# Kernel optimization log

Hardware: AMD Instinct MI355X
Metric: run time of the kernel (lower is better)

## Reference

```python
import jax, jax.numpy as jnp
import numpy as np
import math

D_MODEL, N_HEAD, N_KV_HEAD, MAX_LEN = 2048, 32, 8, 2048
D_K = D_MODEL // N_HEAD
BASE = 10000.0
B, T = 2, 2048


def _rope_tables(seq_len):
    # matches torch Rotary: cos/sin of shape [seq_len, D_K], repeat_interleave(2) over freq dim
    inv_freq = 1.0 / (BASE ** (jnp.arange(0, D_K, 2, dtype=jnp.float32) / D_K))
    t = jnp.arange(seq_len, dtype=jnp.float32)[:, None] * inv_freq  # [T, D_K/2]
    cos = jnp.repeat(jnp.cos(t), 2, axis=-1)  # [T, D_K]
    sin = jnp.repeat(jnp.sin(t), 2, axis=-1)
    return cos, sin


def _rotate_half(x):
    # faithful to source: x1 = even lanes, x2 = odd lanes, concat([-x2, x1], -1)
    x1, x2 = x[..., ::2], x[..., 1::2]
    return jnp.concatenate([-x2, x1], axis=-1)


def _apply_rope(x, cos, sin):
    return x * cos + _rotate_half(x) * sin


def setup_inputs() -> dict:
    key = jax.random.key(0)
    ks = jax.random.split(key, 5)
    s = 1.0 / math.sqrt(D_MODEL)
    x = jax.random.normal(ks[0], (B, T, D_MODEL), dtype=jnp.float32)
    Wq = jax.random.normal(ks[1], (D_MODEL, N_HEAD * D_K), dtype=jnp.float32) * s
    Wk = jax.random.normal(ks[2], (D_MODEL, N_KV_HEAD * D_K), dtype=jnp.float32) * s
    Wv = jax.random.normal(ks[3], (D_MODEL, N_KV_HEAD * D_K), dtype=jnp.float32) * s
    Wo = jax.random.normal(ks[4], (N_HEAD * D_K, D_MODEL), dtype=jnp.float32) * s
    mask = jnp.tril(jnp.ones((T, T), dtype=bool))  # causal
    return {"x": x, "mask": mask, "Wq": Wq, "Wk": Wk, "Wv": Wv, "Wo": Wo}


def reference(x, mask, Wq, Wk, Wv, Wo):
    b, t, _ = x.shape
    g = N_HEAD // N_KV_HEAD
    q = (x @ Wq).reshape(b, t, N_HEAD, D_K).transpose(0, 2, 1, 3)      # [B,H,T,d]
    k = (x @ Wk).reshape(b, t, N_KV_HEAD, D_K).transpose(0, 2, 1, 3)   # [B,Hkv,T,d]
    v = (x @ Wv).reshape(b, t, N_KV_HEAD, D_K).transpose(0, 2, 1, 3)
    cos, sin = _rope_tables(t)
    q = _apply_rope(q, cos, sin)
    k = _apply_rope(k, cos, sin)  # rope before/after repeat is identical per-head
    # grouped attention: q head h attends kv head h // g (repeat_interleave semantics)
    qg = q.reshape(b, N_KV_HEAD, g, t, D_K)
    scores = jnp.einsum("bkgtd,bksd->bkgts", qg, k) / math.sqrt(D_K)
    neg = jnp.finfo(scores.dtype).min
    scores = jnp.where(mask[None, None, None, :, :], scores, neg)
    attn = jax.nn.softmax(scores, axis=-1)
    out = jnp.einsum("bkgts,bksd->bkgtd", attn, v)
    out = out.reshape(b, N_HEAD, t, D_K).transpose(0, 2, 1, 3).reshape(b, t, N_HEAD * D_K)
    return out @ Wo
```

## Files before the change

### kernel.cpp

```cpp
#include <hip/hip_runtime.h>
#include <cstdint>
#include <cstddef>

typedef unsigned short u16;
typedef __attribute__((ext_vector_type(8))) short bf16x8;
typedef __attribute__((ext_vector_type(8))) unsigned short u16x8;
typedef __attribute__((ext_vector_type(4))) unsigned short u16x4;
typedef __attribute__((ext_vector_type(4))) float f32x4;

__device__ __forceinline__ unsigned short f2bf(float f) {
    union { float f; uint32_t u; } c; c.f = f;
    uint32_t u = c.u + 0x7fffu + ((c.u >> 16) & 1u);
    return (unsigned short)(u >> 16);
}
__device__ __forceinline__ float bf2f(unsigned short h) {
    union { uint32_t u; float f; } c; c.u = ((uint32_t)h) << 16;
    return c.f;
}
__device__ __forceinline__ uint32_t pkbf(float a, float b) {
    union { float f; uint32_t u; } x, y; x.f = a; y.f = b;
    return ((x.u + 0x8000u) >> 16) | ((y.u + 0x8000u) & 0xFFFF0000u);
}

#define GLDS16(g, l)                                                               \
    __builtin_amdgcn_global_load_lds((const __attribute__((address_space(1))) void*)(g), \
                                     (__attribute__((address_space(3))) void*)(l), 16, 0, 0)

__global__ __launch_bounds__(256) void cvt_x(const float* __restrict__ src,
                                             u16* __restrict__ dst) {
    int i = blockIdx.x * 256 + threadIdx.x;
    const float4* s = (const float4*)src + (size_t)i * 2;
    float4 a = s[0], b = s[1];
    u16x8 o;
    o[0] = f2bf(a.x); o[1] = f2bf(a.y); o[2] = f2bf(a.z); o[3] = f2bf(a.w);
    o[4] = f2bf(b.x); o[5] = f2bf(b.y); o[6] = f2bf(b.z); o[7] = f2bf(b.w);
    *(u16x8*)(dst + (size_t)i * 8) = o;
}

__global__ __launch_bounds__(256) void tcvt(const float* __restrict__ src,
                                            u16* __restrict__ dst, int C) {
    __shared__ u16 tile[32][33];
    const int t = threadIdx.x;
    const int bx = blockIdx.x, by = blockIdx.y;
    const int tr = t >> 3, tc = (t & 7) << 2;
    float4 f = *(const float4*)&src[(size_t)(by * 32 + tr) * C + bx * 32 + tc];
    tile[tr][tc + 0] = f2bf(f.x); tile[tr][tc + 1] = f2bf(f.y);
    tile[tr][tc + 2] = f2bf(f.z); tile[tr][tc + 3] = f2bf(f.w);
    __syncthreads();
    u16x4 o;
    o[0] = tile[tc + 0][tr]; o[1] = tile[tc + 1][tr];
    o[2] = tile[tc + 2][tr]; o[3] = tile[tc + 3][tr];
    *(u16x4*)&dst[(size_t)(bx * 32 + tr) * 2048 + by * 32 + tc] = o;
}

__global__ __launch_bounds__(256) void tcvt3(const float* __restrict__ Wq,
                                             const float* __restrict__ Wk,
                                             const float* __restrict__ Wv,
                                             u16* __restrict__ dst) {
    __shared__ u16 tile[32][33];
    const int t = threadIdx.x;
    const int bxg = blockIdx.x, by = blockIdx.y;
    const float* src; int C, nb; u16* dbase;
    if (bxg < 64)      { src = Wq; C = 2048; nb = bxg;      dbase = dst; }
    else if (bxg < 80) { src = Wk; C = 512;  nb = bxg - 64; dbase = dst + (size_t)2048 * 2048; }
    else               { src = Wv; C = 512;  nb = bxg - 80; dbase = dst + (size_t)2560 * 2048; }
    const int tr = t >> 3, tc = (t & 7) << 2;
    float4 f = *(const float4*)&src[(size_t)(by * 32 + tr) * C + nb * 32 + tc];
    tile[tr][tc + 0] = f2bf(f.x); tile[tr][tc + 1] = f2bf(f.y);
    tile[tr][tc + 2] = f2bf(f.z); tile[tr][tc + 3] = f2bf(f.w);
    __syncthreads();
    u16x4 o;
    o[0] = tile[tc + 0][tr]; o[1] = tile[tc + 1][tr];
    o[2] = tile[tc + 2][tr]; o[3] = tile[tc + 3][tr];
    *(u16x4*)&dbase[(size_t)(nb * 32 + tr) * 2048 + by * 32 + tc] = o;
}

template <int MODE>
__global__ __launch_bounds__(256) void gemm2(const u16* __restrict__ A,
                                             const u16* __restrict__ Bt,
                                             u16* __restrict__ oq, u16* __restrict__ ok,
                                             u16* __restrict__ ov, float* __restrict__ of) {
    __shared__ u16 As[128 * 32];
    __shared__ u16 Bs[128 * 32];
    const int t = threadIdx.x, w = t >> 6, lane = t & 63;
    const int l15 = lane & 15, quad = lane >> 4;
    const int m0 = blockIdx.y << 7, n0 = blockIdx.x << 7;
    const int K = 2048;
    const int c0 = w * 2, c1 = c0 + 1;
    const int ar0 = c0 * 16 + (lane >> 2), ar1 = c1 * 16 + (lane >> 2);
    const int ac = (lane & 3) << 3;
    const u16* Ap0 = A + (size_t)(m0 + ar0) * K + ac;
    const u16* Ap1 = A + (size_t)(m0 + ar1) * K + ac;
    const u16* Bp0 = Bt + (size_t)(n0 + ar0) * K + ac;
    const u16* Bp1 = Bt + (size_t)(n0 + ar1) * K + ac;
    const int wm = (w >> 1) << 6, wn = (w & 1) << 6;

    f32x4 acc[4][4] = {};

    for (int k0 = 0; k0 < K; k0 += 32) {
        GLDS16(Ap0 + k0, &As[c0 * 512]);
        GLDS16(Ap1 + k0, &As[c1 * 512]);
        GLDS16(Bp0 + k0, &Bs[c0 * 512]);
        GLDS16(Bp1 + k0, &Bs[c1 * 512]);
        __syncthreads();
        bf16x8 a[4], bfr[4];
#pragma unroll
        for (int mt = 0; mt < 4; ++mt)
            a[mt] = *(bf16x8*)&As[(wm + mt * 16 + l15) * 32 + quad * 8];
#pragma unroll
        for (int nt = 0; nt < 4; ++nt)
            bfr[nt] = *(bf16x8*)&Bs[(wn + nt * 16 + l15) * 32 + quad * 8];
#pragma unroll
        for (int mt = 0; mt < 4; ++mt)
#pragma unroll
            for (int nt = 0; nt < 4; ++nt)
                acc[mt][nt] = __builtin_amdgcn_mfma_f32_16x16x32_bf16(a[mt], bfr[nt], acc[mt][nt], 0, 0, 0);
        __syncthreads();
    }

    if constexpr (MODE == 0) {
        const int colbase = n0 + wn;
        const bool isv = (colbase >= 2560);
        float iv[4];
        if (!isv) {
#pragma unroll
            for (int nt = 0; nt < 4; ++nt)
                iv[nt] = exp2f(-0.4152410118609253f * (float)(nt * 8 + (l15 >> 1)));
        }
        const int map1 = (quad << 4) | ((2 * l15 + 1) & 15);
        const int map2 = (quad << 4) | ((2 * l15) & 15);
        const bool lo = (l15 < 8);
#pragma unroll
        for (int mt = 0; mt < 4; ++mt)
#pragma unroll
            for (int r = 0; r < 4; ++r) {
                const int row = m0 + wm + mt * 16 + quad * 4 + r;
                float v0 = acc[mt][0][r], v1 = acc[mt][1][r];
                float v2 = acc[mt][2][r], v3 = acc[mt][3][r];
                float o0 = v0, o1 = v1, o2 = v2, o3 = v3;
                if (!isv) {
                    float g1a = __shfl(v0, map1), g1b = __shfl(v1, map1);
                    float g1c = __shfl(v2, map1), g1d = __shfl(v3, map1);
                    float g2a = __shfl(v0, map2), g2b = __shfl(v1, map2);
                    float g2c = __shfl(v2, map2), g2d = __shfl(v3, map2);
                    float p0 = lo ? g1a : g1b;
                    float p1 = lo ? g1c : g1d;
                    float p2 = lo ? g2a : g2b;
                    float p3 = lo ? g2c : g2d;
                    const float tt = (float)(row & 2047);
                    float sn, cs;
                    __sincosf(tt * iv[0], &sn, &cs); o0 = v0 * cs - p0 * sn;
                    __sincosf(tt * iv[1], &sn, &cs); o1 = v1 * cs - p1 * sn;
                    __sincosf(tt * iv[2], &sn, &cs); o2 = v2 * cs + p2 * sn;
                    __sincosf(tt * iv[3], &sn, &cs); o3 = v3 * cs + p3 * sn;
                }
                float o[4] = {o0, o1, o2, o3};
                if (colbase < 2048) {
#pragma unroll
                    for (int nt = 0; nt < 4; ++nt)
                        oq[(size_t)row * 2048 + colbase + nt * 16 + l15] = f2bf(o[nt]);
                } else if (colbase < 2560) {
#pragma unroll
                    for (int nt = 0; nt < 4; ++nt)
                        ok[(size_t)row * 512 + colbase - 2048 + nt * 16 + l15] = f2bf(o[nt]);
                } else {
#pragma unroll
                    for (int nt = 0; nt < 4; ++nt)
                        ov[(size_t)(colbase - 2560 + nt * 16 + l15) * 4096 + row] = f2bf(o[nt]);
                }
            }
    } else {
#pragma unroll
        for (int mt = 0; mt < 4; ++mt)
#pragma unroll
            for (int nt = 0; nt < 4; ++nt)
#pragma unroll
                for (int r = 0; r < 4; ++r) {
                    int row = m0 + wm + mt * 16 + quad * 4 + r;
                    int col = n0 + wn + nt * 16 + l15;
                    of[(size_t)row * 2048 + col] = acc[mt][nt][r];
                }
    }
}

__global__ __launch_bounds__(256, 3) void attn4(const u16* __restrict__ q,
                                                const u16* __restrict__ k,
                                                const u16* __restrict__ vT,
                                                u16* __restrict__ att) {
    __shared__ u16 Ks[64 * 72];
    __shared__ u16 Vt[64 * 72];
    __shared__ u16 Pw[4][16 * 72];

    const int t = threadIdx.x, w = t >> 6, lane = t & 63;
    const int l15 = lane & 15, quad = lane >> 4;
    const int bx = blockIdx.x, kvh = blockIdx.y, b = blockIdx.z;
    const int h = kvh * 4 + w;
    const size_t rowbase = (size_t)b * 2048;
    const int sr = t >> 2, sd = (t & 3) << 4;
    u16* Pq = &Pw[w][0];
    const float SC = 0.125f * 1.4426950408889634f;

    const u16* kbase = &k[(rowbase + sr) * 512 + kvh * 64 + sd];
    const u16* vbase = &vT[(size_t)(kvh * 64 + sr) * 4096 + rowbase + sd];

    for (int grp = 0; grp < 2; ++grp) {
        const int g = grp ? (63 - bx) : bx;
        const int qbase = g * 32;
        const int ntiles = (g >> 1) + 1;

        bf16x8 aq[2][2];
#pragma unroll
        for (int mt = 0; mt < 2; ++mt)
#pragma unroll
            for (int kc = 0; kc < 2; ++kc)
                aq[mt][kc] = *(const bf16x8*)&q[(rowbase + qbase + mt * 16 + l15) * 2048 +
                                               h * 64 + kc * 32 + quad * 8];

        f32x4 acc[2][4] = {};
        float m_i[2] = {-INFINITY, -INFINITY};
        float l_i[2] = {0.f, 0.f};

        u16x8 pk0 = *(const u16x8*)kbase;
        u16x8 pk1 = *(const u16x8*)(kbase + 8);
        u16x8 pv0 = *(const u16x8*)vbase;
        u16x8 pv1 = *(const u16x8*)(vbase + 8);

        for (int kb = 0; kb < ntiles; ++kb) {
            __syncthreads();
            *(u16x8*)&Ks[sr * 72 + sd]     = pk0;
            *(u16x8*)&Ks[sr * 72 + sd + 8] = pk1;
            *(u16x8*)&Vt[sr * 72 + sd]     = pv0;
            *(u16x8*)&Vt[sr * 72 + sd + 8] = pv1;
            if (kb + 1 < ntiles) {
                const u16* kp = kbase + (size_t)(kb + 1) * 64 * 512;
                pk0 = *(const u16x8*)kp;
                pk1 = *(const u16x8*)(kp + 8);
                const u16* vp = vbase + (size_t)(kb + 1) * 64;
                pv0 = *(const u16x8*)vp;
                pv1 = *(const u16x8*)(vp + 8);
            }
            __syncthreads();

            f32x4 st[2][4] = {};
#pragma unroll
            for (int kt = 0; kt < 4; ++kt) {
                bf16x8 ak0 = *(bf16x8*)&Ks[(kt * 16 + l15) * 72 + quad * 8];
                bf16x8 ak1 = *(bf16x8*)&Ks[(kt * 16 + l15) * 72 + 32 + quad * 8];
                st[0][kt] = __builtin_amdgcn_mfma_f32_16x16x32_bf16(ak0, aq[0][0], st[0][kt], 0, 0, 0);
                st[0][kt] = __builtin_amdgcn_mfma_f32_16x16x32_bf16(ak1, aq[0][1], st[0][kt], 0, 0, 0);
                st[1][kt] = __builtin_amdgcn_mfma_f32_16x16x32_bf16(ak0, aq[1][0], st[1][kt], 0, 0, 0);
                st[1][kt] = __builtin_amdgcn_mfma_f32_16x16x32_bf16(ak1, aq[1][1], st[1][kt], 0, 0, 0);
            }
            const bool diag = (kb == ntiles - 1);

#pragma unroll
            for (int mt = 0; mt < 2; ++mt) {
                float sv[16];
#pragma unroll
                for (int kt = 0; kt < 4; ++kt)
#pragma unroll
                    for (int r = 0; r < 4; ++r) sv[kt * 4 + r] = st[mt][kt][r] * SC;
                if (diag) {
                    const int qg = qbase + mt * 16 + l15;
#pragma unroll
                    for (int kt = 0; kt < 4; ++kt)
#pragma unroll
                        for (int r = 0; r < 4; ++r) {
                            int key = kb * 64 + kt * 16 + quad * 4 + r;
                            if (key > qg) sv[kt * 4 + r] = -INFINITY;
                        }
                }
                float mx = sv[0];
#pragma unroll
                for (int i = 1; i < 16; ++i) mx = fmaxf(mx, sv[i]);
                mx = fmaxf(mx, __shfl_xor(mx, 16));
                mx = fmaxf(mx, __shfl_xor(mx, 32));
                float mnew = fmaxf(m_i[mt], mx);
                float sum = 0.f;
#pragma unroll
                for (int i = 0; i < 16; ++i) {
                    sv[i] = __builtin_amdgcn_exp2f(sv[i] - mnew);
                    sum += sv[i];
                }
                sum += __shfl_xor(sum, 16);
                sum += __shfl_xor(sum, 32);
                float alpha = __builtin_amdgcn_exp2f(m_i[mt] - mnew);
                l_i[mt] = l_i[mt] * alpha + sum;
                m_i[mt] = mnew;

#pragma unroll
                for (int kt = 0; kt < 4; ++kt) {
                    uint2 uu;
                    uu.x = pkbf(sv[kt * 4 + 0], sv[kt * 4 + 1]);
                    uu.y = pkbf(sv[kt * 4 + 2], sv[kt * 4 + 3]);
                    *(uint2*)&Pq[l15 * 72 + kt * 16 + quad * 4] = uu;
                }
                bf16x8 bp0 = *(bf16x8*)&Pq[l15 * 72 + quad * 8];
                bf16x8 bp1 = *(bf16x8*)&Pq[l15 * 72 + 32 + quad * 8];

#pragma unroll
                for (int dt = 0; dt < 4; ++dt) {
                    bf16x8 av0 = *(bf16x8*)&Vt[(dt * 16 + l15) * 72 + quad * 8];
                    bf16x8 av1 = *(bf16x8*)&Vt[(dt * 16 + l15) * 72 + 32 + quad * 8];
#pragma unroll
                    for (int r = 0; r < 4; ++r) acc[mt][dt][r] *= alpha;
                    acc[mt][dt] = __builtin_amdgcn_mfma_f32_16x16x32_bf16(av0, bp0, acc[mt][dt], 0, 0, 0);
                    acc[mt][dt] = __builtin_amdgcn_mfma_f32_16x16x32_bf16(av1, bp1, acc[mt][dt], 0, 0, 0);
                }
            }
        }

#pragma unroll
        for (int mt = 0; mt < 2; ++mt) {
            float inv = 1.0f / l_i[mt];
            size_t row = rowbase + qbase + mt * 16 + l15;
#pragma unroll
            for (int dt = 0; dt < 4; ++dt) {
                uint2 uu;
                uu.x = pkbf(acc[mt][dt][0] * inv, acc[mt][dt][1] * inv);
                uu.y = pkbf(acc[mt][dt][2] * inv, acc[mt][dt][3] * inv);
                *(uint2*)&att[row * 2048 + h * 64 + dt * 16 + quad * 4] = uu;
            }
        }
    }
}

extern "C" void kernel_launch(void* const* d_in, const int* in_sizes, int n_in,
                              void* d_out, int out_size, void* d_ws, size_t ws_size,
                              hipStream_t stream) {
    const float* x  = (const float*)d_in[0];
    const float* Wq = (const float*)d_in[2];
    const float* Wk = (const float*)d_in[3];
    const float* Wv = (const float*)d_in[4];
    const float* Wo = (const float*)d_in[5];
    float* out = (float*)d_out;

    u16* xb = (u16*)d_out;

    u16* q     = (u16*)d_ws;
    u16* kk    = q + (size_t)4096 * 2048;
    u16* vt    = kk + (size_t)4096 * 512;
    u16* wqkvt = vt + (size_t)4096 * 512;
    u16* att   = wqkvt;
    u16* wot   = kk;

    cvt_x<<<4096, 256, 0, stream>>>(x, xb);
    tcvt3<<<dim3(96, 64), 256, 0, stream>>>(Wq, Wk, Wv, wqkvt);
    gemm2<0><<<dim3(24, 32), 256, 0, stream>>>(xb, wqkvt, q, kk, vt, nullptr);
    attn4<<<dim3(32, 8, 2), 256, 0, stream>>>(q, kk, vt, att);
    tcvt<<<dim3(64, 64), 256, 0, stream>>>(Wo, wot, 2048);
    gemm2<1><<<dim3(16, 32), 256, 0, stream>>>(att, wot, nullptr, nullptr, nullptr, out);
}
```

Measured before the change: 332.4 us.

## Process 64-query tiles per wave with lazy softmax rescaling in attention

```diff
diff --git a/kernel.cpp b/kernel.cpp
--- a/kernel.cpp
+++ b/kernel.cpp
@@ -20,6 +20,11 @@
 __device__ __forceinline__ uint32_t pkbf(float a, float b) {
     union { float f; uint32_t u; } x, y; x.f = a; y.f = b;
     return ((x.u + 0x8000u) >> 16) | ((y.u + 0x8000u) & 0xFFFF0000u);
+}
+__device__ __forceinline__ uint32_t cvtpk(float a, float b) {
+    uint32_t r;
+    asm("v_cvt_pk_bf16_f32 %0, %1, %2" : "=v"(r) : "v"(a), "v"(b));
+    return r;
 }
 
 #define GLDS16(g, l)                                                               \
@@ -183,85 +188,92 @@
     }
 }
 
-__global__ __launch_bounds__(256, 3) void attn4(const u16* __restrict__ q,
+__global__ __launch_bounds__(256, 2) void attn5(const u16* __restrict__ q,
                                                 const u16* __restrict__ k,
                                                 const u16* __restrict__ vT,
                                                 u16* __restrict__ att) {
     __shared__ u16 Ks[64 * 72];
     __shared__ u16 Vt[64 * 72];
-    __shared__ u16 Pw[4][16 * 72];
+    __shared__ u16 Pw[4][2][2][16 * 72];
 
     const int t = threadIdx.x, w = t >> 6, lane = t & 63;
     const int l15 = lane & 15, quad = lane >> 4;
-    const int bx = blockIdx.x, kvh = blockIdx.y, b = blockIdx.z;
+    const int x = blockIdx.x, kvh = blockIdx.y, z = blockIdx.z;
+    const int a = z ? (31 - x) : x;
     const int h = kvh * 4 + w;
-    const size_t rowbase = (size_t)b * 2048;
+    const size_t rowbase = (size_t)z * 2048;
     const int sr = t >> 2, sd = (t & 3) << 4;
-    u16* Pq = &Pw[w][0];
     const float SC = 0.125f * 1.4426950408889634f;
 
     const u16* kbase = &k[(rowbase + sr) * 512 + kvh * 64 + sd];
     const u16* vbase = &vT[(size_t)(kvh * 64 + sr) * 4096 + rowbase + sd];
 
-    for (int grp = 0; grp < 2; ++grp) {
-        const int g = grp ? (63 - bx) : bx;
-        const int qbase = g * 32;
-        const int ntiles = (g >> 1) + 1;
-
-        bf16x8 aq[2][2];
-#pragma unroll
-        for (int mt = 0; mt < 2; ++mt)
+    const int ntiles = a + 1;
+    const int qbase0 = a * 64;
+
+    bf16x8 aq[2][2][2];
+#pragma unroll
+    for (int g = 0; g < 2; ++g)
+#pragma unroll
+        for (int m = 0; m < 2; ++m)
 #pragma unroll
             for (int kc = 0; kc < 2; ++kc)
-                aq[mt][kc] = *(const bf16x8*)&q[(rowbase + qbase + mt * 16 + l15) * 2048 +
-                                               h * 64 + kc * 32 + quad * 8];
-
-        f32x4 acc[2][4] = {};
-        float m_i[2] = {-INFINITY, -INFINITY};
-        float l_i[2] = {0.f, 0.f};
-
-        u16x8 pk0 = *(const u16x8*)kbase;
-        u16x8 pk1 = *(const u16x8*)(kbase + 8);
-        u16x8 pv0 = *(const u16x8*)vbase;
-        u16x8 pv1 = *(const u16x8*)(vbase + 8);
-
-        for (int kb = 0; kb < ntiles; ++kb) {
-            __syncthreads();
-            *(u16x8*)&Ks[sr * 72 + sd]     = pk0;
-            *(u16x8*)&Ks[sr * 72 + sd + 8] = pk1;
-            *(u16x8*)&Vt[sr * 72 + sd]     = pv0;
-            *(u16x8*)&Vt[sr * 72 + sd + 8] = pv1;
-            if (kb + 1 < ntiles) {
-                const u16* kp = kbase + (size_t)(kb + 1) * 64 * 512;
-                pk0 = *(const u16x8*)kp;
-                pk1 = *(const u16x8*)(kp + 8);
-                const u16* vp = vbase + (size_t)(kb + 1) * 64;
-                pv0 = *(const u16x8*)vp;
-                pv1 = *(const u16x8*)(vp + 8);
-            }
-            __syncthreads();
-
-            f32x4 st[2][4] = {};
-#pragma unroll
-            for (int kt = 0; kt < 4; ++kt) {
-                bf16x8 ak0 = *(bf16x8*)&Ks[(kt * 16 + l15) * 72 + quad * 8];
-                bf16x8 ak1 = *(bf16x8*)&Ks[(kt * 16 + l15) * 72 + 32 + quad * 8];
-                st[0][kt] = __builtin_amdgcn_mfma_f32_16x16x32_bf16(ak0, aq[0][0], st[0][kt], 0, 0, 0);
-                st[0][kt] = __builtin_amdgcn_mfma_f32_16x16x32_bf16(ak1, aq[0][1], st[0][kt], 0, 0, 0);
-                st[1][kt] = __builtin_amdgcn_mfma_f32_16x16x32_bf16(ak0, aq[1][0], st[1][kt], 0, 0, 0);
-                st[1][kt] = __builtin_amdgcn_mfma_f32_16x16x32_bf16(ak1, aq[1][1], st[1][kt], 0, 0, 0);
-            }
-            const bool diag = (kb == ntiles - 1);
-
-#pragma unroll
-            for (int mt = 0; mt < 2; ++mt) {
+                aq[g][m][kc] = *(const bf16x8*)&q[(rowbase + qbase0 + g * 32 + m * 16 + l15) * 2048 +
+                                                  h * 64 + kc * 32 + quad * 8];
+
+    f32x4 acc[2][2][4] = {};
+    float m_i[2][2] = {{-INFINITY, -INFINITY}, {-INFINITY, -INFINITY}};
+    float l_i[2][2] = {{0.f, 0.f}, {0.f, 0.f}};
+
+    u16x8 pk0 = *(const u16x8*)kbase;
+    u16x8 pk1 = *(const u16x8*)(kbase + 8);
+    u16x8 pv0 = *(const u16x8*)vbase;
+    u16x8 pv1 = *(const u16x8*)(vbase + 8);
+
+    for (int kb = 0; kb < ntiles; ++kb) {
+        __syncthreads();
+        *(u16x8*)&Ks[sr * 72 + sd]     = pk0;
+        *(u16x8*)&Ks[sr * 72 + sd + 8] = pk1;
+        *(u16x8*)&Vt[sr * 72 + sd]     = pv0;
+        *(u16x8*)&Vt[sr * 72 + sd + 8] = pv1;
+        if (kb + 1 < ntiles) {
+            const u16* kp = kbase + (size_t)(kb + 1) * 64 * 512;
+            pk0 = *(const u16x8*)kp;
+            pk1 = *(const u16x8*)(kp + 8);
+            const u16* vp = vbase + (size_t)(kb + 1) * 64;
+            pv0 = *(const u16x8*)vp;
+            pv1 = *(const u16x8*)(vp + 8);
+        }
+        __syncthreads();
+
+        f32x4 st[2][2][4] = {};
+#pragma unroll
+        for (int kt = 0; kt < 4; ++kt) {
+            bf16x8 ak0 = *(bf16x8*)&Ks[(kt * 16 + l15) * 72 + quad * 8];
+            bf16x8 ak1 = *(bf16x8*)&Ks[(kt * 16 + l15) * 72 + 32 + quad * 8];
+#pragma unroll
+            for (int g = 0; g < 2; ++g)
+#pragma unroll
+                for (int m = 0; m < 2; ++m) {
+                    st[g][m][kt] = __builtin_amdgcn_mfma_f32_16x16x32_bf16(ak0, aq[g][m][0], st[g][m][kt], 0, 0, 0);
+                    st[g][m][kt] = __builtin_amdgcn_mfma_f32_16x16x32_bf16(ak1, aq[g][m][1], st[g][m][kt], 0, 0, 0);
+                }
+        }
+        const bool diag = (kb == ntiles - 1);
+
+        float alpha_[2][2];
+        bool  resc[2][2];
+#pragma unroll
+        for (int g = 0; g < 2; ++g)
+#pragma unroll
+            for (int m = 0; m < 2; ++m) {
                 float sv[16];
 #pragma unroll
                 for (int kt = 0; kt < 4; ++kt)
 #pragma unroll
-                    for (int r = 0; r < 4; ++r) sv[kt * 4 + r] = st[mt][kt][r] * SC;
+                    for (int r = 0; r < 4; ++r) sv[kt * 4 + r] = st[g][m][kt][r];
                 if (diag) {
-                    const int qg = qbase + mt * 16 + l15;
+                    const int qg = qbase0 + g * 32 + m * 16 + l15;
 #pragma unroll
                     for (int kt = 0; kt < 4; ++kt)
 #pragma unroll
@@ -275,54 +287,88 @@
                 for (int i = 1; i < 16; ++i) mx = fmaxf(mx, sv[i]);
                 mx = fmaxf(mx, __shfl_xor(mx, 16));
                 mx = fmaxf(mx, __shfl_xor(mx, 32));
-                float mnew = fmaxf(m_i[mt], mx);
+                mx *= SC;
+                const float mold = m_i[g][m];
+                const bool need = __any(mx > mold + 8.f);
+                float al = 1.f;
+                if (need) {
+                    const float mnew = fmaxf(mold, mx);
+                    al = __builtin_amdgcn_exp2f(mold - mnew);
+                    m_i[g][m] = mnew;
+                }
+                const float mu = m_i[g][m];
                 float sum = 0.f;
 #pragma unroll
                 for (int i = 0; i < 16; ++i) {
-                    sv[i] = __builtin_amdgcn_exp2f(sv[i] - mnew);
+                    sv[i] = __builtin_amdgcn_exp2f(fmaf(sv[i], SC, -mu));
                     sum += sv[i];
                 }
                 sum += __shfl_xor(sum, 16);
                 sum += __shfl_xor(sum, 32);
-                float alpha = __builtin_amdgcn_exp2f(m_i[mt] - mnew);
-                l_i[mt] = l_i[mt] * alpha + sum;
-                m_i[mt] = mnew;
-
+                l_i[g][m] = l_i[g][m] * al + sum;
+                alpha_[g][m] = al;
+                resc[g][m] = need;
+
+                u16* Pq = &Pw[w][g][m][0];
 #pragma unroll
                 for (int kt = 0; kt < 4; ++kt) {
                     uint2 uu;
-                    uu.x = pkbf(sv[kt * 4 + 0], sv[kt * 4 + 1]);
-                    uu.y = pkbf(sv[kt * 4 + 2], sv[kt * 4 + 3]);
+                    uu.x = cvtpk(sv[kt * 4 + 0], sv[kt * 4 + 1]);
+                    uu.y = cvtpk(sv[kt * 4 + 2], sv[kt * 4 + 3]);
                     *(uint2*)&Pq[l15 * 72 + kt * 16 + quad * 4] = uu;
                 }
-                bf16x8 bp0 = *(bf16x8*)&Pq[l15 * 72 + quad * 8];
-                bf16x8 bp1 = *(bf16x8*)&Pq[l15 * 72 + 32 + quad * 8];
-
-#pragma unroll
-                for (int dt = 0; dt < 4; ++dt) {
-                    bf16x8 av0 = *(bf16x8*)&Vt[(dt * 16 + l15) * 72 + quad * 8];
-                    bf16x8 av1 = *(bf16x8*)&Vt[(dt * 16 + l15) * 72 + 32 + quad * 8];
-#pragma unroll
-                    for (int r = 0; r < 4; ++r) acc[mt][dt][r] *= alpha;
-                    acc[mt][dt] = __builtin_amdgcn_mfma_f32_16x16x32_bf16(av0, bp0, acc[mt][dt], 0, 0, 0);
-                    acc[mt][dt] = __builtin_amdgcn_mfma_f32_16x16x32_bf16(av1, bp1, acc[mt][dt], 0, 0, 0);
-                }
             }
-        }
-
-#pragma unroll
-        for (int mt = 0; mt < 2; ++mt) {
-            float inv = 1.0f / l_i[mt];
-            size_t row = rowbase + qbase + mt * 16 + l15;
+
+#pragma unroll
+        for (int g = 0; g < 2; ++g)
+#pragma unroll
+            for (int m = 0; m < 2; ++m)
+                if (resc[g][m]) {
+                    const float al = alpha_[g][m];
+#pragma unroll
+                    for (int dt = 0; dt < 4; ++dt)
+#pragma unroll
+                        for (int r = 0; r < 4; ++r) acc[g][m][dt][r] *= al;
+                }
+
+        bf16x8 bp[2][2][2];
+#pragma unroll
+        for (int g = 0; g < 2; ++g)
+#pragma unroll
+            for (int m = 0; m < 2; ++m) {
+                const u16* Pq = &Pw[w][g][m][0];
+                bp[g][m][0] = *(bf16x8*)&Pq[l15 * 72 + quad * 8];
+                bp[g][m][1] = *(bf16x8*)&Pq[l15 * 72 + 32 + quad * 8];
+            }
+
+#pragma unroll
+        for (int dt = 0; dt < 4; ++dt) {
+            bf16x8 av0 = *(bf16x8*)&Vt[(dt * 16 + l15) * 72 + quad * 8];
+            bf16x8 av1 = *(bf16x8*)&Vt[(dt * 16 + l15) * 72 + 32 + quad * 8];
+#pragma unroll
+            for (int g = 0; g < 2; ++g)
+#pragma unroll
+                for (int m = 0; m < 2; ++m) {
+                    acc[g][m][dt] = __builtin_amdgcn_mfma_f32_16x16x32_bf16(av0, bp[g][m][0], acc[g][m][dt], 0, 0, 0);
+                    acc[g][m][dt] = __builtin_amdgcn_mfma_f32_16x16x32_bf16(av1, bp[g][m][1], acc[g][m][dt], 0, 0, 0);
+                }
+        }
+    }
+
+#pragma unroll
+    for (int g = 0; g < 2; ++g)
+#pragma unroll
+        for (int m = 0; m < 2; ++m) {
+            float inv = 1.0f / l_i[g][m];
+            size_t row = rowbase + qbase0 + g * 32 + m * 16 + l15;
 #pragma unroll
             for (int dt = 0; dt < 4; ++dt) {
                 uint2 uu;
-                uu.x = pkbf(acc[mt][dt][0] * inv, acc[mt][dt][1] * inv);
-                uu.y = pkbf(acc[mt][dt][2] * inv, acc[mt][dt][3] * inv);
+                uu.x = cvtpk(acc[g][m][dt][0] * inv, acc[g][m][dt][1] * inv);
+                uu.y = cvtpk(acc[g][m][dt][2] * inv, acc[g][m][dt][3] * inv);
                 *(uint2*)&att[row * 2048 + h * 64 + dt * 16 + quad * 4] = uu;
             }
         }
-    }
 }
 
 extern "C" void kernel_launch(void* const* d_in, const int* in_sizes, int n_in,
@@ -347,7 +393,7 @@
     cvt_x<<<4096, 256, 0, stream>>>(x, xb);
     tcvt3<<<dim3(96, 64), 256, 0, stream>>>(Wq, Wk, Wv, wqkvt);
     gemm2<0><<<dim3(24, 32), 256, 0, stream>>>(xb, wqkvt, q, kk, vt, nullptr);
-    attn4<<<dim3(32, 8, 2), 256, 0, stream>>>(q, kk, vt, att);
+    attn5<<<dim3(32, 8, 2), 256, 0, stream>>>(q, kk, vt, att);
     tcvt<<<dim3(64, 64), 256, 0, stream>>>(Wo, wot, 2048);
     gemm2<1><<<dim3(16, 32), 256, 0, stream>>>(att, wot, nullptr, nullptr, nullptr, out);
 }
```

Result: no change. 331.4 us (-0.3%).
